# Performance work log

Hardware: AMD Instinct MI355X
Metric: run time of the kernel (lower is better)

Reference implementation:

```python
import jax, jax.numpy as jnp
import numpy as np

B, R, C, H, W = 8, 4, 64, 128, 128
RF, E = 256, 8
C2 = 2 * C
K = 3


def setup_inputs() -> dict:
    key = jax.random.key(0)
    ks = jax.random.split(key, 8)
    return {
        "x": jax.random.normal(ks[0], (B, C, H, W), jnp.float32),
        "routing": jax.random.normal(ks[1], (B, R, RF), jnp.float32),
        # nn.Linear(routing_features, num_experts)
        "routing_W": jax.random.normal(ks[2], (RF, E), jnp.float32) * 0.05,
        "routing_b": jnp.zeros((E,), jnp.float32),
        # CondConv2d expert weights: (E, Cout, Cin, k, k)
        "W1": jax.random.normal(ks[3], (E, C2, C, K, K), jnp.float32) * 0.04,
        "prelu_a": jnp.float32(0.25),  # PReLU single shared parameter
        "W2": jax.random.normal(ks[4], (E, C, C2, K, K), jnp.float32) * 0.03,
        # self-routing Linear(2*in_features, num_experts)
        "sr_W": jax.random.normal(ks[5], (C2, E), jnp.float32) * 0.08,
        "sr_b": jnp.zeros((E,), jnp.float32),
        # conv_output: Conv2d(in_features, 1, kernel_size=1) with bias
        "Wout": jax.random.normal(ks[6], (1, C), jnp.float32) * 0.1,
        "bout": jnp.zeros((1,), jnp.float32),
    }


def _prelu(x, a):
    return jnp.where(x >= 0, x, a * x)


def _cond_conv(x, rw, Wexp):
    # x: (B,Cin,H,W); rw: (B,E); Wexp: (E,Cout,Cin,k,k)
    # per-sample mixed kernel, then per-sample conv (vmap over batch)
    w = jnp.einsum('be,eoikl->boikl', rw, Wexp)
    def one(xi, wi):
        return jax.lax.conv_general_dilated(
            xi[None], wi, window_strides=(1, 1), padding=[(1, 1), (1, 1)])[0]
    return jax.vmap(one)(x, w)


def reference(x, routing, routing_W, routing_b, W1, prelu_a, W2, sr_W, sr_b, Wout, bout):
    rw = jax.nn.sigmoid(routing @ routing_W + routing_b)  # (B,R,E)
    rw = jnp.transpose(rw, (1, 0, 2))                     # (R,B,E)

    def per_head(rw_r):
        xc = _prelu(_cond_conv(x, rw_r, W1), prelu_a)      # (B,C2,H,W)
        pooled = xc.mean(axis=(2, 3))                      # adaptive_avg_pool2d(.,1)
        srw = pooled @ sr_W + sr_b                         # no sigmoid (per source)
        xc2 = _prelu(_cond_conv(xc, srw, W2), prelu_a)     # (B,C,H,W)
        out = jnp.einsum('bchw,oc->bohw', xc2, Wout)       # 1x1 conv
        return out + bout[None, :, None, None]             # (B,1,H,W)

    res = jax.vmap(per_head)(rw)                           # (R,B,1,H,W)
    return jnp.transpose(res[:, :, 0], (1, 0, 2, 3))       # (B,R,H,W)
```

## Files before the change

### kernel.cpp

```cpp
#include <hip/hip_runtime.h>
#include <stdint.h>


typedef _Float16 f16_t;
typedef _Float16 f16x8 __attribute__((ext_vector_type(8)));
typedef _Float16 f16x4 __attribute__((ext_vector_type(4)));
typedef float    f32x4 __attribute__((ext_vector_type(4)));

#define B_   8
#define R_   4
#define C_   64
#define C2_  128
#define H_   128
#define W_   128
#define E_   8
#define RF_  256
#define WP_  130
#define HP_  130

__device__ __forceinline__ f32x4 mfma16(f16x8 a, f16x8 b, f32x4 c) {
  return __builtin_amdgcn_mfma_f32_16x16x32_f16(a, b, c, 0, 0, 0);
}

__device__ __forceinline__ void gl16(const f16_t* g, f16_t* l) {
  __builtin_amdgcn_global_load_lds(
      (const __attribute__((address_space(1))) unsigned int*)(const void*)g,
      (__attribute__((address_space(3))) unsigned int*)(void*)l, 16, 0, 0);
}

__device__ __host__ __forceinline__ int sig(int n) { return (n ^ (n >> 2)) & 3; }

__global__ void k_rw(const float* __restrict__ routing, const float* __restrict__ rW,
                     const float* __restrict__ rB, float* __restrict__ rw,
                     float* __restrict__ pooled4) {
  int t = threadIdx.x;
  #pragma unroll
  for (int i = 0; i < 16; ++i) pooled4[i*256 + t] = 0.f;
  int e = t & 7, b = (t >> 3) & 7, r = t >> 6;
  float acc = rB[e];
  for (int f = 0; f < RF_; ++f)
    acc += routing[(b*R_ + r)*RF_ + f] * rW[f*E_ + e];
  rw[(r*B_ + b)*E_ + e] = 1.0f / (1.0f + __expf(-acc));
}

__global__ void k_zero(f16_t* __restrict__ xbt, f16_t* __restrict__ xct,
                       size_t xct_stride) {
  const f16x8 z = {0,0,0,0,0,0,0,0};
  int t = blockIdx.x*256 + threadIdx.x;
  if (t < 16640) {
    int ch = t & 7, u = t >> 3;
    int pix = u % 130; u /= 130;
    int rs = u & 1, b = u >> 1;
    *(f16x8*)&xbt[((size_t)(b*HP_ + rs*129)*WP_ + pix)*C_ + ch*8] = z;
    return;
  }
  t -= 16640;
  if (t < 133120) {
    int ch = t & 15, u = t >> 4;
    int pix = u % 130; u /= 130;
    int rs = u & 1; u >>= 1;
    int b = u & 7, r = u >> 3;
    *(f16x8*)&xct[(size_t)r*xct_stride + ((size_t)(b*HP_ + rs*129)*WP_ + pix)*C2_ + ch*8] = z;
    return;
  }
  t -= 133120;
  if (t < 131072) {
    int ch = t & 15, u = t >> 4;
    int hp = (u & 127) + 1; u >>= 7;
    int cs = u & 1; u >>= 1;
    int b = u & 7, r = u >> 3;
    *(f16x8*)&xct[(size_t)r*xct_stride + ((size_t)(b*HP_ + hp)*WP_ + cs*129)*C2_ + ch*8] = z;
  }
}

__global__ void k_xt(const float* __restrict__ x, f16_t* __restrict__ xbt) {
  int wh = blockIdx.x, h = blockIdx.y, b = blockIdx.z;
  int t = threadIdx.x;
  int w0 = wh * 64;
  __shared__ float tile[64][65];
  #pragma unroll
  for (int rep = 0; rep < 16; ++rep) {
    int idx = rep*256 + t;
    int c = idx >> 6, w = idx & 63;
    tile[c][w] = x[((size_t)(b*C_ + c)*H_ + h)*W_ + w0 + w];
  }
  __syncthreads();
  #pragma unroll
  for (int rep = 0; rep < 16; ++rep) {
    int idx = rep*256 + t;
    int w = idx >> 6, c = idx & 63;
    xbt[((size_t)(b*HP_ + h + 1)*WP_ + (w0 + w + 1))*C_ + c] = (f16_t)tile[c][w];
  }
  if (t < 64) {
    if (wh == 0) xbt[((size_t)(b*HP_ + h + 1)*WP_ + 0)*C_ + t]   = (f16_t)0.0f;
    else         xbt[((size_t)(b*HP_ + h + 1)*WP_ + 129)*C_ + t] = (f16_t)0.0f;
  }
}

__global__ void k_mix1(const float* __restrict__ rw, const float* __restrict__ W1,
                       f16_t* __restrict__ w1m) {
  int gid = blockIdx.x*256 + threadIdx.x;
  int cq4 = gid & 15;
  int s   = (gid >> 4) % 9;
  int t2  = (gid >> 4) / 9;
  int co  = t2 & 127;
  int rb  = t2 >> 7;
  float o0=0.f,o1=0.f,o2=0.f,o3=0.f;
  #pragma unroll
  for (int e = 0; e < E_; ++e) {
    float rv = rw[rb*E_ + e];
    const float* wp = W1 + (size_t)((e*C2_ + co)*C_ + cq4*4)*9 + s;
    o0 += rv*wp[0]; o1 += rv*wp[9]; o2 += rv*wp[18]; o3 += rv*wp[27];
  }
  f16x4 pk; pk[0]=(f16_t)o0; pk[1]=(f16_t)o1; pk[2]=(f16_t)o2; pk[3]=(f16_t)o3;
  int coh = co >> 6, co6 = co & 63;
  int cb  = cq4 >> 3;
  int cqu = (cq4 >> 1) & 3;
  int off = (cq4 & 1) * 4;
  size_t row = ((size_t)(rb*2 + coh)*2 + cb)*64 + co6;
  *(f16x4*)&w1m[row*288 + (size_t)(s*4 + (cqu ^ sig(co6)))*8 + off] = pk;
}

__global__ void k_mix2(const float* __restrict__ pooled, const float* __restrict__ srW,
                       const float* __restrict__ srb, const float* __restrict__ W2,
                       f16_t* __restrict__ w2m, size_t w2m_stride, int r0) {
  const int r = r0 + blockIdx.y;
  const float* pooled_r = pooled + (size_t)r*B_*C2_;
  f16_t* w2m_r = w2m + (size_t)r*w2m_stride;
  __shared__ float sw[64];
  int t = threadIdx.x;
  if (t < 64) {
    int b = t >> 3, e = t & 7;
    float acc = srb[e];
    for (int c = 0; c < C2_; ++c)
      acc += pooled_r[b*C2_ + c] * (1.0f/16384.0f) * srW[c*E_ + e];
    sw[t] = acc;
  }
  __syncthreads();
  int gid = blockIdx.x*256 + t;
  int c2q = gid & 31;
  int s   = (gid >> 5) % 9;
  int t2  = (gid >> 5) / 9;
  int co  = t2 & 63;
  int b   = t2 >> 6;
  float o0=0.f,o1=0.f,o2=0.f,o3=0.f;
  #pragma unroll
  for (int e = 0; e < E_; ++e) {
    float rv = sw[b*E_ + e];
    const float* wp = W2 + (size_t)((e*C_ + co)*C2_ + c2q*4)*9 + s;
    o0 += rv*wp[0]; o1 += rv*wp[9]; o2 += rv*wp[18]; o3 += rv*wp[27];
  }
  f16x4 pk; pk[0]=(f16_t)o0; pk[1]=(f16_t)o1; pk[2]=(f16_t)o2; pk[3]=(f16_t)o3;
  int it  = c2q >> 3;
  int cqu = (c2q >> 1) & 3;
  int off = (c2q & 1) * 4;
  size_t row = ((size_t)b*4 + it)*64 + co;
  *(f16x4*)&w2m_r[row*288 + (size_t)(s*4 + (cqu ^ sig(co)))*8 + off] = pk;
}

__global__ __launch_bounds__(256, 2) void k_conv1(
    const f16_t* __restrict__ xbt, const f16_t* __restrict__ w1m,
    const float* __restrict__ pa, f16_t* __restrict__ xct, size_t xct_stride,
    float* __restrict__ pooled, int r0)
{
  const int bx = blockIdx.x;
  const int b = bx & 7, h0 = (bx >> 3) << 1;
  const int coh = blockIdx.y;
  const int r = r0 + blockIdx.z;
  f16_t* xct_r = xct + (size_t)r*xct_stride;
  float* pooled_r = pooled + (size_t)r*B_*C2_;
  const int tid = threadIdx.x;
  const int lane = tid & 63;
  const int wid = tid >> 6;
  const int wrow = wid >> 1, wph = wid & 1;
  const int l15 = lane & 15, l4 = lane >> 4;
  __shared__ __align__(16) f16_t lA[64*288];
  __shared__ __align__(16) f16_t lB[2080*8];

  const int xorA = (l4 ^ sig(l15)) << 4;
  int bbase[3];
  #pragma unroll
  for (int dw = 0; dw < 3; ++dw) {
    int P0 = wph*64 + dw + l15;
    bbase[dw] = P0*64 + ((l4 ^ sig(P0)) << 4);
  }

  const f32x4 vzero = {0.f,0.f,0.f,0.f};
  f32x4 acc[4][4];
  #pragma unroll
  for (int i=0;i<4;++i)
    #pragma unroll
    for (int j=0;j<4;++j) acc[i][j] = vzero;

  const int rb = r*B_ + b;
  const f16_t* w1base = w1m + ((size_t)(rb*2 + coh)*2)*64*288;
  const f16_t* xb = xbt + ((size_t)(b*HP_ + h0))*WP_*C_;

  for (int cb = 0; cb < 2; ++cb) {
    __syncthreads();
    #pragma unroll
    for (int k = 0; k < 9; ++k) {
      int u = k*256 + tid;
      gl16(w1base + (size_t)cb*64*288 + (size_t)u*8, &lA[u*8]);
    }
    #pragma unroll
    for (int k = 0; k < 8; ++k) {
      int u = k*256 + tid;
      int row = u / 520, rem = u - row*520;
      int pix = rem >> 2, cq = (rem & 3) ^ sig(pix);
      gl16(xb + ((size_t)row*WP_ + pix)*C_ + cb*32 + cq*8, &lB[u*8]);
    }
    if (tid < 32) {
      int u = 2048 + tid;
      int rem = u - 1560;
      int pix = rem >> 2, cq = (rem & 3) ^ sig(pix);
      gl16(xb + ((size_t)3*WP_ + pix)*C_ + cb*32 + cq*8, &lB[u*8]);
    }
    __syncthreads();
    __builtin_amdgcn_s_setprio(1);
    #pragma unroll
    for (int dh = 0; dh < 3; ++dh) {
      #pragma unroll
      for (int dw = 0; dw < 3; ++dw) {
        const int s = dh*3 + dw;
        f16x8 af[4], bf[4];
        #pragma unroll
        for (int fm = 0; fm < 4; ++fm)
          af[fm] = *(const f16x8*)((const char*)lA + (fm*16 + l15)*576 + s*64 + xorA);
        #pragma unroll
        for (int fn = 0; fn < 4; ++fn)
          bf[fn] = *(const f16x8*)((const char*)lB + (wrow + dh)*8320 + bbase[dw] + fn*1024);
        #pragma unroll
        for (int fm = 0; fm < 4; ++fm)
          #pragma unroll
          for (int fn = 0; fn < 4; ++fn)
            acc[fm][fn] = mfma16(af[fm], bf[fn], acc[fm][fn]);
      }
    }
    __builtin_amdgcn_s_setprio(0);
  }

  const float a = pa[0];
  float ps[4][4];
  #pragma unroll
  for (int fm=0;fm<4;++fm)
    #pragma unroll
    for (int j=0;j<4;++j) ps[fm][j] = 0.f;
  #pragma unroll
  for (int fm = 0; fm < 4; ++fm)
    #pragma unroll
    for (int fn = 0; fn < 4; ++fn)
      #pragma unroll
      for (int j = 0; j < 4; ++j) {
        float v = acc[fm][fn][j];
        v = (v >= 0.f) ? v : a*v;
        acc[fm][fn][j] = v;
        ps[fm][j] += v;
      }
  #pragma unroll
  for (int fm = 0; fm < 4; ++fm)
    #pragma unroll
    for (int j = 0; j < 4; ++j) {
      float s = ps[fm][j];
      s += __shfl_xor(s, 1, 64);
      s += __shfl_xor(s, 2, 64);
      s += __shfl_xor(s, 4, 64);
      s += __shfl_xor(s, 8, 64);
      ps[fm][j] = s;
    }
  __syncthreads();
  f16_t* lso = lA;
  float* lps = (float*)lB;
  const int prow = wrow*128 + wph*64;
  #pragma unroll
  for (int fm = 0; fm < 4; ++fm)
    #pragma unroll
    for (int fn = 0; fn < 4; ++fn) {
      f16x4 pk;
      #pragma unroll
      for (int j = 0; j < 4; ++j) pk[j] = (f16_t)acc[fm][fn][j];
      *(f16x4*)&lso[(prow + fn*16 + l15)*72 + fm*16 + l4*4] = pk;
    }
  if (l15 == 0) {
    #pragma unroll
    for (int fm = 0; fm < 4; ++fm)
      #pragma unroll
      for (int j = 0; j < 4; ++j)
        lps[wid*64 + fm*16 + l4*4 + j] = ps[fm][j];
  }
  __syncthreads();
  #pragma unroll
  for (int p = 0; p < 8; ++p) {
    int i = p*256 + tid;
    int pl = i >> 3, q = i & 7;
    int row = pl >> 7, pix = pl & 127;
    uint4 v = *(const uint4*)&lso[pl*72 + q*8];
    *(uint4*)(xct_r + ((size_t)(b*HP_ + h0 + row + 1)*WP_ + pix + 1)*C2_ + coh*64 + q*8) = v;
  }
  if (tid < 64) {
    float s = lps[tid] + lps[64 + tid] + lps[128 + tid] + lps[192 + tid];
    atomicAdd(&pooled_r[b*C2_ + coh*64 + tid], s);
  }
}

__global__ __launch_bounds__(256, 2) void k_conv2(
    const f16_t* __restrict__ xct, size_t xct_stride,
    const f16_t* __restrict__ w2m, size_t w2m_stride,
    const float* __restrict__ pa, const float* __restrict__ Wout,
    const float* __restrict__ bout, float* __restrict__ out, int r0)
{
  const int bx = blockIdx.x;
  const int b = bx & 7, h0 = (bx >> 3) << 1;
  const int r = r0 + blockIdx.y;
  const int tid = threadIdx.x;
  const int lane = tid & 63;
  const int wid = tid >> 6;
  const int wrow = wid >> 1, wph = wid & 1;
  const int l15 = lane & 15, l4 = lane >> 4;
  __shared__ __align__(16) f16_t lA[64*288];
  __shared__ __align__(16) f16_t lB[2080*8];

  const int xorA = (l4 ^ sig(l15)) << 4;
  int bbase[3];
  #pragma unroll
  for (int dw = 0; dw < 3; ++dw) {
    int P0 = wph*64 + dw + l15;
    bbase[dw] = P0*64 + ((l4 ^ sig(P0)) << 4);
  }

  const f32x4 vzero = {0.f,0.f,0.f,0.f};
  f32x4 acc[4][4];
  #pragma unroll
  for (int i=0;i<4;++i)
    #pragma unroll
    for (int j=0;j<4;++j) acc[i][j] = vzero;

  const f16_t* w2base = w2m + (size_t)r*w2m_stride + (size_t)b*4*64*288;
  const f16_t* xb = xct + (size_t)r*xct_stride + ((size_t)(b*HP_ + h0))*WP_*C2_;

  for (int it = 0; it < 4; ++it) {
    __syncthreads();
    #pragma unroll
    for (int k = 0; k < 9; ++k) {
      int u = k*256 + tid;
      gl16(w2base + (size_t)it*64*288 + (size_t)u*8, &lA[u*8]);
    }
    #pragma unroll
    for (int k = 0; k < 8; ++k) {
      int u = k*256 + tid;
      int row = u / 520, rem = u - row*520;
      int pix = rem >> 2, cq = (rem & 3) ^ sig(pix);
      gl16(xb + ((size_t)row*WP_ + pix)*C2_ + it*32 + cq*8, &lB[u*8]);
    }
    if (tid < 32) {
      int u = 2048 + tid;
      int rem = u - 1560;
      int pix = rem >> 2, cq = (rem & 3) ^ sig(pix);
      gl16(xb + ((size_t)3*WP_ + pix)*C2_ + it*32 + cq*8, &lB[u*8]);
    }
    __syncthreads();
    __builtin_amdgcn_s_setprio(1);
    #pragma unroll
    for (int dh = 0; dh < 3; ++dh) {
      #pragma unroll
      for (int dw = 0; dw < 3; ++dw) {
        const int s = dh*3 + dw;
        f16x8 af[4], bf[4];
        #pragma unroll
        for (int fm = 0; fm < 4; ++fm)
          af[fm] = *(const f16x8*)((const char*)lA + (fm*16 + l15)*576 + s*64 + xorA);
        #pragma unroll
        for (int fn = 0; fn < 4; ++fn)
          bf[fn] = *(const f16x8*)((const char*)lB + (wrow + dh)*8320 + bbase[dw] + fn*1024);
        #pragma unroll
        for (int fm = 0; fm < 4; ++fm)
          #pragma unroll
          for (int fn = 0; fn < 4; ++fn)
            acc[fm][fn] = mfma16(af[fm], bf[fn], acc[fm][fn]);
      }
    }
    __builtin_amdgcn_s_setprio(0);
  }

  const float a  = pa[0];
  const float bo = bout[0];
  float wr_[4][4];
  #pragma unroll
  for (int fm = 0; fm < 4; ++fm)
    #pragma unroll
    for (int j = 0; j < 4; ++j)
      wr_[fm][j] = Wout[fm*16 + l4*4 + j];
  float* orow = out + ((size_t)((b*R_ + r)*H_ + h0 + wrow))*W_;
  #pragma unroll
  for (int fn = 0; fn < 4; ++fn) {
    float s = 0.f;
    #pragma unroll
    for (int fm = 0; fm < 4; ++fm)
      #pragma unroll
      for (int j = 0; j < 4; ++j) {
        float v = acc[fm][fn][j];
        v = (v >= 0.f) ? v : a*v;
        s += wr_[fm][j]*v;
      }
    s += __shfl_xor(s, 16, 64);
    s += __shfl_xor(s, 32, 64);
    if (lane < 16)
      orow[wph*64 + fn*16 + lane] = s + bo;
  }
}

extern "C" void kernel_launch(void* const* d_in, const int* in_sizes, int n_in,
                              void* d_out, int out_size, void* d_ws, size_t ws_size,
                              hipStream_t stream) {
  (void)in_sizes; (void)n_in; (void)out_size;
  const float* x       = (const float*)d_in[0];
  const float* routing = (const float*)d_in[1];
  const float* rW      = (const float*)d_in[2];
  const float* rB      = (const float*)d_in[3];
  const float* W1      = (const float*)d_in[4];
  const float* pa      = (const float*)d_in[5];
  const float* W2      = (const float*)d_in[6];
  const float* srW     = (const float*)d_in[7];
  const float* srb     = (const float*)d_in[8];
  const float* Wout    = (const float*)d_in[9];
  const float* bout    = (const float*)d_in[10];
  float* out = (float*)d_out;

  const size_t xct_one = (size_t)B_*HP_*WP_*C2_;
  const size_t w2m_one = (size_t)2048*288;
  const size_t need_fused = 17305600ull + 4718592ull + 4*xct_one*2 + 4*w2m_one*2 + 32768ull;
  const bool fused = (ws_size >= need_fused);
  const int ncopies = fused ? 4 : 1;
  const size_t xs = fused ? xct_one : 0;
  const size_t ws2 = fused ? w2m_one : 0;

  char* ws = (char*)d_ws;
  size_t off = 0;
  f16_t* xbt = (f16_t*)(ws + off); off += (size_t)B_*HP_*WP_*C_*2;
  f16_t* w1m = (f16_t*)(ws + off); off += (size_t)8192*288*2;
  f16_t* xct = (f16_t*)(ws + off); off += xct_one*2*ncopies;
  f16_t* w2m = (f16_t*)(ws + off); off += w2m_one*2*ncopies;
  float* rw     = (float*)(ws + off); off += (size_t)R_*B_*E_*4;
  float* pooled = (float*)(ws + off); off += (size_t)R_*B_*C2_*4;

  k_rw  <<<1, 256, 0, stream>>>(routing, rW, rB, rw, pooled);
  k_zero<<<1097, 256, 0, stream>>>(xbt, xct, xs);
  k_xt  <<<dim3(2, H_, B_), 256, 0, stream>>>(x, xbt);
  k_mix1<<<2304, 256, 0, stream>>>(rw, W1, w1m);
  if (fused) {
    k_conv1<<<dim3(512, 2, 4), 256, 0, stream>>>(xbt, w1m, pa, xct, xs, pooled, 0);
    k_mix2 <<<dim3(576, 4), 256, 0, stream>>>(pooled, srW, srb, W2, w2m, ws2, 0);
    k_conv2<<<dim3(512, 4), 256, 0, stream>>>(xct, xs, w2m, ws2, pa, Wout, bout, out, 0);
  } else {
    for (int r = 0; r < R_; ++r) {
      k_conv1<<<dim3(512, 2, 1), 256, 0, stream>>>(xbt, w1m, pa, xct, xs, pooled, r);
      k_mix2 <<<dim3(576, 1), 256, 0, stream>>>(pooled, srW, srb, W2, w2m, ws2, r);
      k_conv2<<<dim3(512, 1), 256, 0, stream>>>(xct, xs, w2m, ws2, pa, Wout, bout, out, r);
    }
  }
}
```

Before: 242.8 us.

## Enlarge conv tiles to 512-thread blocks covering more rows and all output channels

Both implicit-GEMM convolution kernels move from 256-thread blocks to 512-thread blocks. conv1 now covers 4 output rows and all 128 channels per block, with the W1 mixed-weight layout reordered to match. conv2 now covers 8 rows per block, and each warp computes a full 128-pixel row with 8 N-fragments. This reduces the halo and weight reloading per output and raises MFMA work per LDS fragment load. In exchange it uses more registers (32 accumulators per lane) and more LDS per block, which may lower occupancy. The conv1 epilogue is restaged row by row through LDS and does the pooled atomics per wave.

```diff
diff --git a/kernel.cpp b/kernel.cpp
--- a/kernel.cpp
+++ b/kernel.cpp
@@ -113,12 +113,11 @@
     o0 += rv*wp[0]; o1 += rv*wp[9]; o2 += rv*wp[18]; o3 += rv*wp[27];
   }
   f16x4 pk; pk[0]=(f16_t)o0; pk[1]=(f16_t)o1; pk[2]=(f16_t)o2; pk[3]=(f16_t)o3;
-  int coh = co >> 6, co6 = co & 63;
   int cb  = cq4 >> 3;
-  int cqu = (cq4 >> 1) & 3;
+  int q   = (cq4 >> 1) & 3;
   int off = (cq4 & 1) * 4;
-  size_t row = ((size_t)(rb*2 + coh)*2 + cb)*64 + co6;
-  *(f16x4*)&w1m[row*288 + (size_t)(s*4 + (cqu ^ sig(co6)))*8 + off] = pk;
+  size_t row = ((size_t)(rb*2 + cb)*128 + co);
+  *(f16x4*)&w1m[row*288 + (size_t)(s*4 + (q ^ sig(co)))*8 + off] = pk;
 }
 
 __global__ void k_mix2(const float* __restrict__ pooled, const float* __restrict__ srW,
@@ -152,90 +151,85 @@
   }
   f16x4 pk; pk[0]=(f16_t)o0; pk[1]=(f16_t)o1; pk[2]=(f16_t)o2; pk[3]=(f16_t)o3;
   int it  = c2q >> 3;
-  int cqu = (c2q >> 1) & 3;
+  int q   = (c2q >> 1) & 3;
   int off = (c2q & 1) * 4;
   size_t row = ((size_t)b*4 + it)*64 + co;
-  *(f16x4*)&w2m_r[row*288 + (size_t)(s*4 + (cqu ^ sig(co)))*8 + off] = pk;
-}
-
-__global__ __launch_bounds__(256, 2) void k_conv1(
+  *(f16x4*)&w2m_r[row*288 + (size_t)(s*4 + (q ^ sig(co)))*8 + off] = pk;
+}
+
+__global__ __launch_bounds__(512, 2) void k_conv1(
     const f16_t* __restrict__ xbt, const f16_t* __restrict__ w1m,
     const float* __restrict__ pa, f16_t* __restrict__ xct, size_t xct_stride,
     float* __restrict__ pooled, int r0)
 {
   const int bx = blockIdx.x;
-  const int b = bx & 7, h0 = (bx >> 3) << 1;
-  const int coh = blockIdx.y;
+  const int b = bx & 7, h0 = (bx >> 3) << 2;
   const int r = r0 + blockIdx.z;
-  f16_t* xct_r = xct + (size_t)r*xct_stride;
+  f16_t* xct_r = xct + (size_t)blockIdx.z*xct_stride;
   float* pooled_r = pooled + (size_t)r*B_*C2_;
   const int tid = threadIdx.x;
   const int lane = tid & 63;
   const int wid = tid >> 6;
-  const int wrow = wid >> 1, wph = wid & 1;
+  const int wrow = wid >> 1, wm = wid & 1;
   const int l15 = lane & 15, l4 = lane >> 4;
-  __shared__ __align__(16) f16_t lA[64*288];
-  __shared__ __align__(16) f16_t lB[2080*8];
+  __shared__ __align__(16) f16_t lA[128*288];
+  __shared__ __align__(16) f16_t lB[3120*8];
 
   const int xorA = (l4 ^ sig(l15)) << 4;
-  int bbase[3];
-  #pragma unroll
-  for (int dw = 0; dw < 3; ++dw) {
-    int P0 = wph*64 + dw + l15;
-    bbase[dw] = P0*64 + ((l4 ^ sig(P0)) << 4);
-  }
-
-  const f32x4 vzero = {0.f,0.f,0.f,0.f};
-  f32x4 acc[4][4];
+  int xorB[3];
+  #pragma unroll
+  for (int dw = 0; dw < 3; ++dw) xorB[dw] = (l4 ^ sig(l15 + dw)) << 4;
+
+  f32x4 acc[4][8];
   #pragma unroll
   for (int i=0;i<4;++i)
     #pragma unroll
-    for (int j=0;j<4;++j) acc[i][j] = vzero;
+    for (int j=0;j<8;++j) acc[i][j] = (f32x4){0.f,0.f,0.f,0.f};
 
   const int rb = r*B_ + b;
-  const f16_t* w1base = w1m + ((size_t)(rb*2 + coh)*2)*64*288;
+  const f16_t* w1base = w1m + (size_t)rb*2*128*288;
   const f16_t* xb = xbt + ((size_t)(b*HP_ + h0))*WP_*C_;
 
   for (int cb = 0; cb < 2; ++cb) {
     __syncthreads();
     #pragma unroll
     for (int k = 0; k < 9; ++k) {
-      int u = k*256 + tid;
-      gl16(w1base + (size_t)cb*64*288 + (size_t)u*8, &lA[u*8]);
-    }
-    #pragma unroll
-    for (int k = 0; k < 8; ++k) {
-      int u = k*256 + tid;
-      int row = u / 520, rem = u - row*520;
+      int u = k*512 + tid;
+      gl16(w1base + (size_t)cb*128*288 + (size_t)u*8, &lA[u*8]);
+    }
+    #pragma unroll
+    for (int k = 0; k < 6; ++k) {
+      int u = k*512 + tid;
+      int lr = u / 520, rem = u - lr*520;
       int pix = rem >> 2, cq = (rem & 3) ^ sig(pix);
-      gl16(xb + ((size_t)row*WP_ + pix)*C_ + cb*32 + cq*8, &lB[u*8]);
-    }
-    if (tid < 32) {
-      int u = 2048 + tid;
-      int rem = u - 1560;
+      gl16(xb + ((size_t)lr*WP_ + pix)*C_ + cb*32 + cq*8, &lB[u*8]);
+    }
+    if (tid < 48) {
+      int u = 3072 + tid;
+      int rem = u - 2600;
       int pix = rem >> 2, cq = (rem & 3) ^ sig(pix);
-      gl16(xb + ((size_t)3*WP_ + pix)*C_ + cb*32 + cq*8, &lB[u*8]);
+      gl16(xb + ((size_t)5*WP_ + pix)*C_ + cb*32 + cq*8, &lB[u*8]);
     }
     __syncthreads();
     __builtin_amdgcn_s_setprio(1);
     #pragma unroll
-    for (int dh = 0; dh < 3; ++dh) {
-      #pragma unroll
-      for (int dw = 0; dw < 3; ++dw) {
-        const int s = dh*3 + dw;
-        f16x8 af[4], bf[4];
+    for (int s = 0; s < 9; ++s) {
+      const int dh = s / 3, dw = s % 3;
+      f16x8 af[4];
+      #pragma unroll
+      for (int fm = 0; fm < 4; ++fm)
+        af[fm] = *(const f16x8*)((const char*)lA
+                   + (wm*64 + fm*16 + l15)*576 + s*64 + xorA);
+      const char* bbase = (const char*)lB + (wrow + dh)*8320 + (l15 + dw)*64 + xorB[dw];
+      f16x8 bf[8];
+      #pragma unroll
+      for (int fn = 0; fn < 8; ++fn)
+        bf[fn] = *(const f16x8*)(bbase + fn*1024);
+      #pragma unroll
+      for (int fm = 0; fm < 4; ++fm)
         #pragma unroll
-        for (int fm = 0; fm < 4; ++fm)
-          af[fm] = *(const f16x8*)((const char*)lA + (fm*16 + l15)*576 + s*64 + xorA);
-        #pragma unroll
-        for (int fn = 0; fn < 4; ++fn)
-          bf[fn] = *(const f16x8*)((const char*)lB + (wrow + dh)*8320 + bbase[dw] + fn*1024);
-        #pragma unroll
-        for (int fm = 0; fm < 4; ++fm)
-          #pragma unroll
-          for (int fn = 0; fn < 4; ++fn)
-            acc[fm][fn] = mfma16(af[fm], bf[fn], acc[fm][fn]);
-      }
+        for (int fn = 0; fn < 8; ++fn)
+          acc[fm][fn] = mfma16(af[fm], bf[fn], acc[fm][fn]);
     }
     __builtin_amdgcn_s_setprio(0);
   }
@@ -249,7 +243,7 @@
   #pragma unroll
   for (int fm = 0; fm < 4; ++fm)
     #pragma unroll
-    for (int fn = 0; fn < 4; ++fn)
+    for (int fn = 0; fn < 8; ++fn)
       #pragma unroll
       for (int j = 0; j < 4; ++j) {
         float v = acc[fm][fn][j];
@@ -266,118 +260,108 @@
       s += __shfl_xor(s, 2, 64);
       s += __shfl_xor(s, 4, 64);
       s += __shfl_xor(s, 8, 64);
-      ps[fm][j] = s;
-    }
-  __syncthreads();
-  f16_t* lso = lA;
-  float* lps = (float*)lB;
-  const int prow = wrow*128 + wph*64;
-  #pragma unroll
-  for (int fm = 0; fm < 4; ++fm)
-    #pragma unroll
-    for (int fn = 0; fn < 4; ++fn) {
-      f16x4 pk;
-      #pragma unroll
-      for (int j = 0; j < 4; ++j) pk[j] = (f16_t)acc[fm][fn][j];
-      *(f16x4*)&lso[(prow + fn*16 + l15)*72 + fm*16 + l4*4] = pk;
-    }
-  if (l15 == 0) {
-    #pragma unroll
-    for (int fm = 0; fm < 4; ++fm)
-      #pragma unroll
-      for (int j = 0; j < 4; ++j)
-        lps[wid*64 + fm*16 + l4*4 + j] = ps[fm][j];
-  }
-  __syncthreads();
-  #pragma unroll
-  for (int p = 0; p < 8; ++p) {
-    int i = p*256 + tid;
-    int pl = i >> 3, q = i & 7;
-    int row = pl >> 7, pix = pl & 127;
-    uint4 v = *(const uint4*)&lso[pl*72 + q*8];
-    *(uint4*)(xct_r + ((size_t)(b*HP_ + h0 + row + 1)*WP_ + pix + 1)*C2_ + coh*64 + q*8) = v;
-  }
-  if (tid < 64) {
-    float s = lps[tid] + lps[64 + tid] + lps[128 + tid] + lps[192 + tid];
-    atomicAdd(&pooled_r[b*C2_ + coh*64 + tid], s);
-  }
-}
-
-__global__ __launch_bounds__(256, 2) void k_conv2(
+      if (l15 == 0)
+        atomicAdd(&pooled_r[b*C2_ + wm*64 + fm*16 + l4*4 + j], s);
+    }
+  #pragma unroll
+  for (int t4 = 0; t4 < 4; ++t4) {
+    __syncthreads();
+    if (wrow == t4) {
+      #pragma unroll
+      for (int fm = 0; fm < 4; ++fm)
+        #pragma unroll
+        for (int fn = 0; fn < 8; ++fn) {
+          f16x4 pk;
+          #pragma unroll
+          for (int j = 0; j < 4; ++j) pk[j] = (f16_t)acc[fm][fn][j];
+          int pix = fn*16 + l15;
+          *(f16x4*)((char*)lB + pix*336 + wm*160 + (fm*16 + l4*4)*2) = pk;
+        }
+    }
+    __syncthreads();
+    #pragma unroll
+    for (int k = 0; k < 4; ++k) {
+      int idx = tid + 512*k;
+      int pix = idx >> 4, u = idx & 15;
+      f16x8 v = *(const f16x8*)((const char*)lB + pix*336 + u*16 + ((u >= 8) ? 32 : 0));
+      *(f16x8*)(xct_r + ((size_t)(b*HP_ + h0 + t4 + 1)*WP_ + pix + 1)*C2_ + u*8) = v;
+    }
+  }
+}
+
+__global__ __launch_bounds__(512, 2) void k_conv2(
     const f16_t* __restrict__ xct, size_t xct_stride,
     const f16_t* __restrict__ w2m, size_t w2m_stride,
     const float* __restrict__ pa, const float* __restrict__ Wout,
     const float* __restrict__ bout, float* __restrict__ out, int r0)
 {
   const int bx = blockIdx.x;
-  const int b = bx & 7, h0 = (bx >> 3) << 1;
+  const int b = bx & 7, h0 = (bx >> 3) << 3;
   const int r = r0 + blockIdx.y;
   const int tid = threadIdx.x;
   const int lane = tid & 63;
   const int wid = tid >> 6;
-  const int wrow = wid >> 1, wph = wid & 1;
   const int l15 = lane & 15, l4 = lane >> 4;
   __shared__ __align__(16) f16_t lA[64*288];
-  __shared__ __align__(16) f16_t lB[2080*8];
+  __shared__ __align__(16) f16_t lB[5200*8];
 
   const int xorA = (l4 ^ sig(l15)) << 4;
-  int bbase[3];
-  #pragma unroll
-  for (int dw = 0; dw < 3; ++dw) {
-    int P0 = wph*64 + dw + l15;
-    bbase[dw] = P0*64 + ((l4 ^ sig(P0)) << 4);
-  }
-
-  const f32x4 vzero = {0.f,0.f,0.f,0.f};
-  f32x4 acc[4][4];
+  int xorB[3];
+  #pragma unroll
+  for (int dw = 0; dw < 3; ++dw) xorB[dw] = (l4 ^ sig(l15 + dw)) << 4;
+
+  f32x4 acc[4][8];
   #pragma unroll
   for (int i=0;i<4;++i)
     #pragma unroll
-    for (int j=0;j<4;++j) acc[i][j] = vzero;
+    for (int j=0;j<8;++j) acc[i][j] = (f32x4){0.f,0.f,0.f,0.f};
 
   const f16_t* w2base = w2m + (size_t)r*w2m_stride + (size_t)b*4*64*288;
-  const f16_t* xb = xct + (size_t)r*xct_stride + ((size_t)(b*HP_ + h0))*WP_*C2_;
+  const f16_t* xb = xct + (size_t)blockIdx.y*xct_stride + ((size_t)(b*HP_ + h0))*WP_*C2_;
 
   for (int it = 0; it < 4; ++it) {
     __syncthreads();
     #pragma unroll
-    for (int k = 0; k < 9; ++k) {
-      int u = k*256 + tid;
+    for (int k = 0; k < 4; ++k) {
+      int u = k*512 + tid;
       gl16(w2base + (size_t)it*64*288 + (size_t)u*8, &lA[u*8]);
     }
-    #pragma unroll
-    for (int k = 0; k < 8; ++k) {
-      int u = k*256 + tid;
-      int row = u / 520, rem = u - row*520;
+    if (tid < 256) {
+      int u = 2048 + tid;
+      gl16(w2base + (size_t)it*64*288 + (size_t)u*8, &lA[u*8]);
+    }
+    #pragma unroll
+    for (int k = 0; k < 10; ++k) {
+      int u = k*512 + tid;
+      int lr = u / 520, rem = u - lr*520;
       int pix = rem >> 2, cq = (rem & 3) ^ sig(pix);
-      gl16(xb + ((size_t)row*WP_ + pix)*C2_ + it*32 + cq*8, &lB[u*8]);
-    }
-    if (tid < 32) {
-      int u = 2048 + tid;
-      int rem = u - 1560;
+      gl16(xb + ((size_t)lr*WP_ + pix)*C2_ + it*32 + cq*8, &lB[u*8]);
+    }
+    if (tid < 80) {
+      int u = 5120 + tid;
+      int rem = u - 4680;
       int pix = rem >> 2, cq = (rem & 3) ^ sig(pix);
-      gl16(xb + ((size_t)3*WP_ + pix)*C2_ + it*32 + cq*8, &lB[u*8]);
+      gl16(xb + ((size_t)9*WP_ + pix)*C2_ + it*32 + cq*8, &lB[u*8]);
     }
     __syncthreads();
     __builtin_amdgcn_s_setprio(1);
     #pragma unroll
-    for (int dh = 0; dh < 3; ++dh) {
-      #pragma unroll
-      for (int dw = 0; dw < 3; ++dw) {
-        const int s = dh*3 + dw;
-        f16x8 af[4], bf[4];
+    for (int s = 0; s < 9; ++s) {
+      const int dh = s / 3, dw = s % 3;
+      f16x8 af[4];
+      #pragma unroll
+      for (int fm = 0; fm < 4; ++fm)
+        af[fm] = *(const f16x8*)((const char*)lA + (fm*16 + l15)*576 + s*64 + xorA);
+      const char* bbase = (const char*)lB + (wid + dh)*8320 + (l15 + dw)*64 + xorB[dw];
+      f16x8 bf[8];
+      #pragma unroll
+      for (int fn = 0; fn < 8; ++fn)
+        bf[fn] = *(const f16x8*)(bbase + fn*1024);
+      #pragma unroll
+      for (int fm = 0; fm < 4; ++fm)
         #pragma unroll
-        for (int fm = 0; fm < 4; ++fm)
-          af[fm] = *(const f16x8*)((const char*)lA + (fm*16 + l15)*576 + s*64 + xorA);
-        #pragma unroll
-        for (int fn = 0; fn < 4; ++fn)
-          bf[fn] = *(const f16x8*)((const char*)lB + (wrow + dh)*8320 + bbase[dw] + fn*1024);
-        #pragma unroll
-        for (int fm = 0; fm < 4; ++fm)
-          #pragma unroll
-          for (int fn = 0; fn < 4; ++fn)
-            acc[fm][fn] = mfma16(af[fm], bf[fn], acc[fm][fn]);
-      }
+        for (int fn = 0; fn < 8; ++fn)
+          acc[fm][fn] = mfma16(af[fm], bf[fn], acc[fm][fn]);
     }
     __builtin_amdgcn_s_setprio(0);
   }
@@ -390,9 +374,9 @@
     #pragma unroll
     for (int j = 0; j < 4; ++j)
       wr_[fm][j] = Wout[fm*16 + l4*4 + j];
-  float* orow = out + ((size_t)((b*R_ + r)*H_ + h0 + wrow))*W_;
-  #pragma unroll
-  for (int fn = 0; fn < 4; ++fn) {
+  float* orow = out + ((size_t)((b*R_ + r)*H_ + h0 + wid))*W_;
+  #pragma unroll
+  for (int fn = 0; fn < 8; ++fn) {
     float s = 0.f;
     #pragma unroll
     for (int fm = 0; fm < 4; ++fm)
@@ -405,7 +389,7 @@
     s += __shfl_xor(s, 16, 64);
     s += __shfl_xor(s, 32, 64);
     if (lane < 16)
-      orow[wph*64 + fn*16 + lane] = s + bo;
+      orow[fn*16 + lane] = s + bo;
   }
 }
 
@@ -448,14 +432,14 @@
   k_xt  <<<dim3(2, H_, B_), 256, 0, stream>>>(x, xbt);
   k_mix1<<<2304, 256, 0, stream>>>(rw, W1, w1m);
   if (fused) {
-    k_conv1<<<dim3(512, 2, 4), 256, 0, stream>>>(xbt, w1m, pa, xct, xs, pooled, 0);
+    k_conv1<<<dim3(256, 1, 4), 512, 0, stream>>>(xbt, w1m, pa, xct, xs, pooled, 0);
     k_mix2 <<<dim3(576, 4), 256, 0, stream>>>(pooled, srW, srb, W2, w2m, ws2, 0);
-    k_conv2<<<dim3(512, 4), 256, 0, stream>>>(xct, xs, w2m, ws2, pa, Wout, bout, out, 0);
+    k_conv2<<<dim3(128, 4), 512, 0, stream>>>(xct, xs, w2m, ws2, pa, Wout, bout, out, 0);
   } else {
     for (int r = 0; r < R_; ++r) {
-      k_conv1<<<dim3(512, 2, 1), 256, 0, stream>>>(xbt, w1m, pa, xct, xs, pooled, r);
+      k_conv1<<<dim3(256, 1, 1), 512, 0, stream>>>(xbt, w1m, pa, xct, xs, pooled, r);
       k_mix2 <<<dim3(576, 1), 256, 0, stream>>>(pooled, srW, srb, W2, w2m, ws2, r);
-      k_conv2<<<dim3(512, 1), 256, 0, stream>>>(xct, xs, w2m, ws2, pa, Wout, bout, out, r);
-    }
-  }
-}
+      k_conv2<<<dim3(128, 1), 512, 0, stream>>>(xct, xs, w2m, ws2, pa, Wout, bout, out, r);
+    }
+  }
+}
```

New measurement: 271.6 us. 1.12x slower.
